# Performance work log

Hardware: AMD Instinct MI355X
Metric: run time of the kernel (lower is better)

## Reference

```python
import jax, jax.numpy as jnp
import numpy as np

DIM = 384
NUM_HEADS = 6
HEAD_DIM = DIM // NUM_HEADS
SCALE = HEAD_DIM ** -0.5


def setup_inputs() -> dict:
    key = jax.random.key(0)
    k_x, k_qkvw, k_qkvb, k_pw, k_pb = jax.random.split(key, 5)
    B, N, C = 8, 2048, DIM
    x = jax.random.normal(k_x, (B, N, C), dtype=jnp.float32)
    # nn.Linear weights stored as (out, in); apply as x @ W.T + b
    s = 1.0 / np.sqrt(C)
    qkv_w = jax.random.uniform(k_qkvw, (3 * C, C), minval=-s, maxval=s, dtype=jnp.float32)
    qkv_b = jax.random.uniform(k_qkvb, (3 * C,), minval=-s, maxval=s, dtype=jnp.float32)
    proj_w = jax.random.uniform(k_pw, (C, C), minval=-s, maxval=s, dtype=jnp.float32)
    proj_b = jax.random.uniform(k_pb, (C,), minval=-s, maxval=s, dtype=jnp.float32)
    return {"x": x, "qkv_w": qkv_w, "qkv_b": qkv_b, "proj_w": proj_w,
            "proj_b": proj_b, "h": 64, "w": 32}


def reference(x, qkv_w, qkv_b, proj_w, proj_b, h, w):
    B, N, C = x.shape
    H, D = NUM_HEADS, HEAD_DIM
    qkv = x @ qkv_w.T + qkv_b              # [B, N, 3C]
    qkv = qkv.reshape(B, N, 3, H, D)
    q = qkv[:, :, 0].transpose(0, 2, 1, 3) * SCALE  # [B, H, N, D]
    k = qkv[:, :, 1].transpose(0, 2, 1, 3)
    v = qkv[:, :, 2].transpose(0, 2, 1, 3)
    attn = jnp.einsum('bhnd,bhmd->bhnm', q, k)      # [B, H, N, N]
    attn = jax.nn.softmax(attn, axis=-1)
    out = jnp.einsum('bhnm,bhmd->bhnd', attn, v)    # [B, H, N, D]
    out = out.transpose(0, 2, 1, 3).reshape(B, N, C)
    return out @ proj_w.T + proj_b
```

## Files before the change

### kernel.cpp

```cpp
#include <hip/hip_runtime.h>

typedef __attribute__((ext_vector_type(8))) short bf16x8;
typedef __attribute__((ext_vector_type(4))) float f32x4;
typedef __attribute__((ext_vector_type(16))) float f32x16;
typedef __attribute__((ext_vector_type(4))) unsigned int u32x4;

#define DIMC 384
#define NHEADS 6
#define HDIM 64
#define BATCH 8
#define SEQ 2048
#define TOKENS (BATCH*SEQ)
#define QKV_OUT (3*DIMC)

__device__ __forceinline__ unsigned short f2bf(float f) {
  unsigned int u = __float_as_uint(f);
  u += 0x7fffu + ((u >> 16) & 1u);
  return (unsigned short)(u >> 16);
}

__device__ __forceinline__ unsigned int cvt_pk_bf16(float a, float b) {
  unsigned int r;
  asm volatile("v_cvt_pk_bf16_f32 %0, %1, %2" : "=v"(r) : "v"(a), "v"(b));
  return r;
}

__device__ __forceinline__ void async_load16(const void* g, void* l) {
  __builtin_amdgcn_global_load_lds(
      (const __attribute__((address_space(1))) unsigned int*)g,
      (__attribute__((address_space(3))) unsigned int*)l, 16, 0, 0);
}

__global__ void cast_bf16_kernel(const float* __restrict__ in,
                                 unsigned short* __restrict__ out, int n4) {
  int i = blockIdx.x * blockDim.x + threadIdx.x;
  int stride = gridDim.x * blockDim.x;
  for (; i < n4; i += stride) {
    float4 v = ((const float4*)in)[i];
    ushort4 o;
    o.x = f2bf(v.x); o.y = f2bf(v.y); o.z = f2bf(v.z); o.w = f2bf(v.w);
    ((ushort4*)out)[i] = o;
  }
}

__global__ __launch_bounds__(256) void qkv_gemm_kernel(
    const unsigned short* __restrict__ A,
    const unsigned short* __restrict__ W,
    const float* __restrict__ bias,
    unsigned short* __restrict__ Qb,
    unsigned short* __restrict__ Kb,
    unsigned short* __restrict__ Vtb) {
  __shared__ unsigned short As[128*32];
  __shared__ unsigned short Bs[128*32];
  const int tid = threadIdx.x;
  const int w = tid >> 6, l = tid & 63;
  const int wm = w >> 1, wn = w & 1;
  const int q4 = l >> 4, r15 = l & 15;
  const int m0 = blockIdx.y * 128;
  const int n0 = blockIdx.x * 128;

  f32x4 acc[4][4];
#pragma unroll
  for (int i = 0; i < 4; i++)
#pragma unroll
    for (int j = 0; j < 4; j++) acc[i][j] = f32x4{0.f, 0.f, 0.f, 0.f};

  const int arow = tid >> 2;
  const int achk = tid & 3;
  for (int kt = 0; kt < 384; kt += 32) {
    __syncthreads();
#pragma unroll
    for (int cc = 0; cc < 2; ++cc) {
      int row = cc * 64 + arow;
      async_load16(A + (size_t)(m0 + row) * 384 + kt + achk * 8,
                   (char*)As + cc * 4096 + w * 1024);
      async_load16(W + (size_t)(n0 + row) * 384 + kt + achk * 8,
                   (char*)Bs + cc * 4096 + w * 1024);
    }
    __syncthreads();
    bf16x8 a[4], b[4];
#pragma unroll
    for (int mi = 0; mi < 4; mi++)
      a[mi] = *(const bf16x8*)(As + (wm*64 + mi*16 + r15)*32 + q4*8);
#pragma unroll
    for (int ni = 0; ni < 4; ni++)
      b[ni] = *(const bf16x8*)(Bs + (wn*64 + ni*16 + r15)*32 + q4*8);
#pragma unroll
    for (int mi = 0; mi < 4; mi++)
#pragma unroll
      for (int ni = 0; ni < 4; ni++)
        acc[mi][ni] = __builtin_amdgcn_mfma_f32_16x16x32_bf16(
            a[mi], b[ni], acc[mi][ni], 0, 0, 0);
  }
  const int c3 = blockIdx.x / 3;
  const int nrel0 = (blockIdx.x % 3) * 128 + wn * 64;
  if (c3 == 2) {
#pragma unroll
    for (int ni = 0; ni < 4; ni++) {
      int ncol = nrel0 + ni*16 + r15;
      float bv = bias[n0 + wn*64 + ni*16 + r15];
      int h = ncol >> 6, d = ncol & 63;
#pragma unroll
      for (int mi = 0; mi < 4; mi++) {
        int m = m0 + wm*64 + mi*16 + 4*q4;
        int bb = m >> 11, t = m & 2047;
        ushort4 pk;
        pk.x = f2bf(acc[mi][ni][0] + bv);
        pk.y = f2bf(acc[mi][ni][1] + bv);
        pk.z = f2bf(acc[mi][ni][2] + bv);
        pk.w = f2bf(acc[mi][ni][3] + bv);
        *(ushort4*)(Vtb + ((size_t)(bb*NHEADS + h)*HDIM + d)*SEQ + t) = pk;
      }
    }
  } else {
    unsigned short* D = (c3 == 0) ? Qb : Kb;
    const float scale = (c3 == 0) ? 0.125f * 1.4426950408889634f : 1.0f;
#pragma unroll
    for (int ni = 0; ni < 4; ni++) {
      int ncol = nrel0 + ni*16 + r15;
      float bv = bias[n0 + wn*64 + ni*16 + r15];
      int h = ncol >> 6, d = ncol & 63;
#pragma unroll
      for (int mi = 0; mi < 4; mi++) {
#pragma unroll
        for (int reg = 0; reg < 4; reg++) {
          int m = m0 + wm*64 + mi*16 + 4*q4 + reg;
          int bb = m >> 11, t = m & 2047;
          float v = (acc[mi][ni][reg] + bv) * scale;
          D[((size_t)(bb*NHEADS + h)*SEQ + t)*HDIM + d] = f2bf(v);
        }
      }
    }
  }
}

__global__ __launch_bounds__(256, 3) void flash_kernel(
    const unsigned short* __restrict__ Q, const unsigned short* __restrict__ K,
    const unsigned short* __restrict__ Vt, unsigned short* __restrict__ O2) {
  __shared__ unsigned short Ks[2][64*64];
  __shared__ unsigned short Vs[2][64*64];
  const int tid = threadIdx.x;
  const int w = tid >> 6, l = tid & 63;
  const int hl = l >> 5, l31 = l & 31, l7 = l & 7;
  const int wg = blockIdx.x;
  const int logical = (wg & 7) * 96 + (wg >> 3);
  const int qt = logical & 15, bh = logical >> 4;
  const unsigned short* Qp = Q  + (size_t)bh * SEQ * HDIM;
  const unsigned short* Kp = K  + (size_t)bh * SEQ * HDIM;
  const unsigned short* Vp = Vt + (size_t)bh * HDIM * SEQ;

  const int qrow = qt*128 + w*32 + l31;
  bf16x8 qf[4];
#pragma unroll
  for (int ks = 0; ks < 4; ks++)
    qf[ks] = *(const bf16x8*)(Qp + (size_t)qrow*HDIM + ks*16 + hl*8);

  const int srow = w*8 + (l >> 3);
  const int sch  = l7 ^ (l >> 3);
  const unsigned short* Ksrc = Kp + (size_t)srow*HDIM + sch*8;
  const unsigned short* Vsrc = Vp + (size_t)srow*SEQ  + sch*8;
  char* kdst = (char*)&Ks[0][0] + w*1024;
  char* vdst = (char*)&Vs[0][0] + w*1024;

  int rdoff[4];
#pragma unroll
  for (int ks = 0; ks < 4; ks++)
    rdoff[ks] = l31*128 + (((ks*2 + hl) ^ l7) << 4);

  f32x16 o0 = {}, o1 = {};
  float l_run = 0.f;

  async_load16(Ksrc,           kdst);
  async_load16(Ksrc + 32*HDIM, kdst + 4096);
  async_load16(Vsrc,           vdst);
  async_load16(Vsrc + 32*SEQ,  vdst + 4096);

#pragma unroll 2
  for (int kt = 0; kt < 32; ++kt) {
    const int buf = kt & 1;
    const unsigned short* ksb = &Ks[buf][0];
    const unsigned short* vsb = &Vs[buf][0];
    if (kt < 31) {
      const unsigned short* ks_ = Ksrc + (size_t)(kt+1)*64*HDIM;
      const unsigned short* vs_ = Vsrc + (size_t)(kt+1)*64;
      char* kd = kdst + (buf^1)*8192;
      char* vd = vdst + (buf^1)*8192;
      async_load16(ks_,           kd);
      async_load16(ks_ + 32*HDIM, kd + 4096);
      async_load16(vs_,           vd);
      async_load16(vs_ + 32*SEQ,  vd + 4096);
      asm volatile("s_waitcnt vmcnt(4)" ::: "memory");
    } else {
      asm volatile("s_waitcnt vmcnt(0)" ::: "memory");
    }
    __builtin_amdgcn_s_barrier();
    asm volatile("" ::: "memory");

    f32x16 s0 = {}, s1 = {};
    __builtin_amdgcn_s_setprio(1);
#pragma unroll
    for (int ks = 0; ks < 4; ks++) {
      bf16x8 kf0 = *(const bf16x8*)((const char*)ksb + rdoff[ks]);
      bf16x8 kf1 = *(const bf16x8*)((const char*)ksb + 4096 + rdoff[ks]);
      s0 = __builtin_amdgcn_mfma_f32_32x32x16_bf16(kf0, qf[ks], s0, 0, 0, 0);
      s1 = __builtin_amdgcn_mfma_f32_32x32x16_bf16(kf1, qf[ks], s1, 0, 0, 0);
    }
    __builtin_amdgcn_s_setprio(0);

    unsigned int Y[2][4][2];
    float lsum = 0.f;
#pragma unroll
    for (int h = 0; h < 4; h++) {
      float a0 = __builtin_amdgcn_exp2f(s0[4*h+0]);
      float a1 = __builtin_amdgcn_exp2f(s0[4*h+1]);
      float a2 = __builtin_amdgcn_exp2f(s0[4*h+2]);
      float a3 = __builtin_amdgcn_exp2f(s0[4*h+3]);
      lsum += (a0+a1)+(a2+a3);
      Y[0][h][0] = cvt_pk_bf16(a0, a1);
      Y[0][h][1] = cvt_pk_bf16(a2, a3);
      float b0 = __builtin_amdgcn_exp2f(s1[4*h+0]);
      float b1 = __builtin_amdgcn_exp2f(s1[4*h+1]);
      float b2 = __builtin_amdgcn_exp2f(s1[4*h+2]);
      float b3 = __builtin_amdgcn_exp2f(s1[4*h+3]);
      lsum += (b0+b1)+(b2+b3);
      Y[1][h][0] = cvt_pk_bf16(b0, b1);
      Y[1][h][1] = cvt_pk_bf16(b2, b3);
    }
    l_run += lsum;

    bf16x8 pa[4];
#pragma unroll
    for (int ksl = 0; ksl < 4; ksl++) {
      const int kb = ksl >> 1, P2 = ksl & 1;
      unsigned int x0 = Y[kb][2*P2+0][0], x1 = Y[kb][2*P2+0][1];
      unsigned int y0 = Y[kb][2*P2+1][0], y1 = Y[kb][2*P2+1][1];
      asm volatile("v_permlane32_swap_b32 %0, %1" : "+v"(x0), "+v"(y0));
      asm volatile("v_permlane32_swap_b32 %0, %1" : "+v"(x1), "+v"(y1));
      u32x4 t; t[0] = x0; t[1] = x1; t[2] = y0; t[3] = y1;
      union { u32x4 u; bf16x8 b; } cvt; cvt.u = t;
      pa[ksl] = cvt.b;
    }

    __builtin_amdgcn_s_setprio(1);
#pragma unroll
    for (int ksl = 0; ksl < 4; ksl++) {
      bf16x8 vf0 = *(const bf16x8*)((const char*)vsb + rdoff[ksl]);
      bf16x8 vf1 = *(const bf16x8*)((const char*)vsb + 4096 + rdoff[ksl]);
      o0 = __builtin_amdgcn_mfma_f32_32x32x16_bf16(pa[ksl], vf0, o0, 0, 0, 0);
      o1 = __builtin_amdgcn_mfma_f32_32x32x16_bf16(pa[ksl], vf1, o1, 0, 0, 0);
    }
    __builtin_amdgcn_s_setprio(0);
    asm volatile("s_waitcnt lgkmcnt(0)" ::: "memory");
    __builtin_amdgcn_s_barrier();
    asm volatile("" ::: "memory");
  }

  l_run += __shfl_xor(l_run, 32, 64);
  const float linv = 1.0f / l_run;
  const int b = bh / NHEADS, h = bh % NHEADS;
#pragma unroll
  for (int reg = 0; reg < 16; reg++) {
    const int qr = (reg & 3) + 8*(reg >> 2) + 4*hl;
    const float lr = __shfl(linv, qr, 64);
    const int t = qt*128 + w*32 + qr;
    unsigned short* dst = O2 + ((size_t)(b*SEQ + t))*DIMC + h*HDIM;
    dst[l31]      = f2bf(o0[reg] * lr);
    dst[32 + l31] = f2bf(o1[reg] * lr);
  }
}

__global__ __launch_bounds__(256) void proj_gemm_kernel(
    const unsigned short* __restrict__ A,
    const unsigned short* __restrict__ W,
    const float* __restrict__ bias,
    float* __restrict__ out) {
  __shared__ unsigned short As[128*32];
  __shared__ unsigned short Bs[128*32];
  const int tid = threadIdx.x;
  const int w = tid >> 6, l = tid & 63;
  const int wm = w >> 1, wn = w & 1;
  const int q4 = l >> 4, r15 = l & 15;
  const int m0 = blockIdx.y * 128;
  const int n0 = blockIdx.x * 128;

  f32x4 acc[4][4];
#pragma unroll
  for (int i = 0; i < 4; i++)
#pragma unroll
    for (int j = 0; j < 4; j++) acc[i][j] = f32x4{0.f, 0.f, 0.f, 0.f};

  const int arow = tid >> 2;
  const int achk = tid & 3;
  for (int kt = 0; kt < 384; kt += 32) {
    __syncthreads();
#pragma unroll
    for (int cc = 0; cc < 2; ++cc) {
      int row = cc * 64 + arow;
      async_load16(A + (size_t)(m0 + row) * 384 + kt + achk * 8,
                   (char*)As + cc * 4096 + w * 1024);
      async_load16(W + (size_t)(n0 + row) * 384 + kt + achk * 8,
                   (char*)Bs + cc * 4096 + w * 1024);
    }
    __syncthreads();
    bf16x8 a[4], b[4];
#pragma unroll
    for (int mi = 0; mi < 4; mi++)
      a[mi] = *(const bf16x8*)(As + (wm*64 + mi*16 + r15)*32 + q4*8);
#pragma unroll
    for (int ni = 0; ni < 4; ni++)
      b[ni] = *(const bf16x8*)(Bs + (wn*64 + ni*16 + r15)*32 + q4*8);
#pragma unroll
    for (int mi = 0; mi < 4; mi++)
#pragma unroll
      for (int ni = 0; ni < 4; ni++)
        acc[mi][ni] = __builtin_amdgcn_mfma_f32_16x16x32_bf16(
            a[mi], b[ni], acc[mi][ni], 0, 0, 0);
  }
#pragma unroll
  for (int ni = 0; ni < 4; ni++) {
    int ncol = n0 + wn*64 + ni*16 + r15;
    float bv = bias[ncol];
#pragma unroll
    for (int mi = 0; mi < 4; mi++) {
#pragma unroll
      for (int reg = 0; reg < 4; reg++) {
        int m = m0 + wm*64 + mi*16 + 4*q4 + reg;
        out[(size_t)m * DIMC + ncol] = acc[mi][ni][reg] + bv;
      }
    }
  }
}

extern "C" void kernel_launch(void* const* d_in, const int* in_sizes, int n_in,
                              void* d_out, int out_size, void* d_ws, size_t ws_size,
                              hipStream_t stream) {
  const float* x      = (const float*)d_in[0];
  const float* qkv_w  = (const float*)d_in[1];
  const float* qkv_b  = (const float*)d_in[2];
  const float* proj_w = (const float*)d_in[3];
  const float* proj_b = (const float*)d_in[4];
  float* out = (float*)d_out;

  unsigned short* xbf   = (unsigned short*)d_ws;
  unsigned short* wqkv  = xbf   + (size_t)TOKENS * DIMC;
  unsigned short* wproj = wqkv  + (size_t)QKV_OUT * DIMC;
  unsigned short* Qb    = wproj + (size_t)DIMC * DIMC;
  unsigned short* Kb    = Qb    + (size_t)TOKENS * DIMC;
  unsigned short* Vtb   = Kb    + (size_t)TOKENS * DIMC;
  unsigned short* A2    = Vtb   + (size_t)TOKENS * DIMC;

  cast_bf16_kernel<<<2048, 256, 0, stream>>>(x, xbf, TOKENS * DIMC / 4);
  cast_bf16_kernel<<<432, 256, 0, stream>>>(qkv_w, wqkv, QKV_OUT * DIMC / 4);
  cast_bf16_kernel<<<144, 256, 0, stream>>>(proj_w, wproj, DIMC * DIMC / 4);
  qkv_gemm_kernel<<<dim3(9, 128), 256, 0, stream>>>(xbf, wqkv, qkv_b, Qb, Kb, Vtb);
  flash_kernel<<<768, 256, 0, stream>>>(Qb, Kb, Vtb, A2);
  proj_gemm_kernel<<<dim3(3, 128), 256, 0, stream>>>(A2, wproj, proj_b, out);
}
```

Before: 127.5 us.

## Double-buffer GEMMs, shrink flash blocks, fuse casts, retile projection

```diff
diff --git a/kernel.cpp b/kernel.cpp
--- a/kernel.cpp
+++ b/kernel.cpp
@@ -31,15 +31,26 @@
       (__attribute__((address_space(3))) unsigned int*)l, 16, 0, 0);
 }
 
-__global__ void cast_bf16_kernel(const float* __restrict__ in,
-                                 unsigned short* __restrict__ out, int n4) {
+#define N4_X   (TOKENS*DIMC/4)
+#define N4_W1  (QKV_OUT*DIMC/4)
+#define N4_W2  (DIMC*DIMC/4)
+__global__ void cast3_kernel(const float* __restrict__ x,
+                             const float* __restrict__ w1,
+                             const float* __restrict__ w2,
+                             unsigned short* __restrict__ ox,
+                             unsigned short* __restrict__ o1,
+                             unsigned short* __restrict__ o2) {
   int i = blockIdx.x * blockDim.x + threadIdx.x;
-  int stride = gridDim.x * blockDim.x;
-  for (; i < n4; i += stride) {
-    float4 v = ((const float4*)in)[i];
+  const int stride = gridDim.x * blockDim.x;
+  for (; i < N4_X + N4_W1 + N4_W2; i += stride) {
+    const float* src; unsigned short* dst; int j = i;
+    if (j < N4_X)            { src = x;  dst = ox; }
+    else if (j < N4_X+N4_W1) { j -= N4_X; src = w1; dst = o1; }
+    else                     { j -= N4_X+N4_W1; src = w2; dst = o2; }
+    float4 v = ((const float4*)src)[j];
     ushort4 o;
     o.x = f2bf(v.x); o.y = f2bf(v.y); o.z = f2bf(v.z); o.w = f2bf(v.w);
-    ((ushort4*)out)[i] = o;
+    ((ushort4*)dst)[j] = o;
   }
 }
 
@@ -50,8 +61,8 @@
     unsigned short* __restrict__ Qb,
     unsigned short* __restrict__ Kb,
     unsigned short* __restrict__ Vtb) {
-  __shared__ unsigned short As[128*32];
-  __shared__ unsigned short Bs[128*32];
+  __shared__ unsigned short As[2][128*32];
+  __shared__ unsigned short Bs[2][128*32];
   const int tid = threadIdx.x;
   const int w = tid >> 6, l = tid & 63;
   const int wm = w >> 1, wn = w & 1;
@@ -65,32 +76,49 @@
 #pragma unroll
     for (int j = 0; j < 4; j++) acc[i][j] = f32x4{0.f, 0.f, 0.f, 0.f};
 
-  const int arow = tid >> 2;
-  const int achk = tid & 3;
-  for (int kt = 0; kt < 384; kt += 32) {
-    __syncthreads();
-#pragma unroll
-    for (int cc = 0; cc < 2; ++cc) {
-      int row = cc * 64 + arow;
-      async_load16(A + (size_t)(m0 + row) * 384 + kt + achk * 8,
-                   (char*)As + cc * 4096 + w * 1024);
-      async_load16(W + (size_t)(n0 + row) * 384 + kt + achk * 8,
-                   (char*)Bs + cc * 4096 + w * 1024);
-    }
-    __syncthreads();
+  const int arow = l >> 2;
+  const int achk = l & 3;
+  const unsigned short* Asrc = A + (size_t)(m0 + w*16 + arow) * 384 + achk * 8;
+  const unsigned short* Wsrc = W + (size_t)(n0 + w*16 + arow) * 384 + achk * 8;
+
+#pragma unroll
+  for (int cc = 0; cc < 2; ++cc) {
+    async_load16(Asrc + cc*64*384, (char*)As[0] + cc*4096 + w*1024);
+    async_load16(Wsrc + cc*64*384, (char*)Bs[0] + cc*4096 + w*1024);
+  }
+
+  for (int kt = 0; kt < 12; ++kt) {
+    const int buf = kt & 1;
+    if (kt < 11) {
+#pragma unroll
+      for (int cc = 0; cc < 2; ++cc) {
+        async_load16(Asrc + (kt+1)*32 + cc*64*384, (char*)As[buf^1] + cc*4096 + w*1024);
+        async_load16(Wsrc + (kt+1)*32 + cc*64*384, (char*)Bs[buf^1] + cc*4096 + w*1024);
+      }
+      asm volatile("s_waitcnt vmcnt(4)" ::: "memory");
+    } else {
+      asm volatile("s_waitcnt vmcnt(0)" ::: "memory");
+    }
+    __builtin_amdgcn_s_barrier();
+    asm volatile("" ::: "memory");
     bf16x8 a[4], b[4];
 #pragma unroll
     for (int mi = 0; mi < 4; mi++)
-      a[mi] = *(const bf16x8*)(As + (wm*64 + mi*16 + r15)*32 + q4*8);
+      a[mi] = *(const bf16x8*)(&As[buf][(wm*64 + mi*16 + r15)*32 + q4*8]);
 #pragma unroll
     for (int ni = 0; ni < 4; ni++)
-      b[ni] = *(const bf16x8*)(Bs + (wn*64 + ni*16 + r15)*32 + q4*8);
+      b[ni] = *(const bf16x8*)(&Bs[buf][(wn*64 + ni*16 + r15)*32 + q4*8]);
+    __builtin_amdgcn_s_setprio(1);
 #pragma unroll
     for (int mi = 0; mi < 4; mi++)
 #pragma unroll
       for (int ni = 0; ni < 4; ni++)
         acc[mi][ni] = __builtin_amdgcn_mfma_f32_16x16x32_bf16(
             a[mi], b[ni], acc[mi][ni], 0, 0, 0);
+    __builtin_amdgcn_s_setprio(0);
+    asm volatile("s_waitcnt lgkmcnt(0)" ::: "memory");
+    __builtin_amdgcn_s_barrier();
+    asm volatile("" ::: "memory");
   }
   const int c3 = blockIdx.x / 3;
   const int nrel0 = (blockIdx.x % 3) * 128 + wn * 64;
@@ -134,7 +162,7 @@
   }
 }
 
-__global__ __launch_bounds__(256, 3) void flash_kernel(
+__global__ __launch_bounds__(128) void flash_kernel(
     const unsigned short* __restrict__ Q, const unsigned short* __restrict__ K,
     const unsigned short* __restrict__ Vt, unsigned short* __restrict__ O2) {
   __shared__ unsigned short Ks[2][64*64];
@@ -143,24 +171,23 @@
   const int w = tid >> 6, l = tid & 63;
   const int hl = l >> 5, l31 = l & 31, l7 = l & 7;
   const int wg = blockIdx.x;
-  const int logical = (wg & 7) * 96 + (wg >> 3);
-  const int qt = logical & 15, bh = logical >> 4;
+  const int logical = (wg & 7) * 192 + (wg >> 3);
+  const int qt = logical & 31, bh = logical >> 5;
   const unsigned short* Qp = Q  + (size_t)bh * SEQ * HDIM;
   const unsigned short* Kp = K  + (size_t)bh * SEQ * HDIM;
   const unsigned short* Vp = Vt + (size_t)bh * HDIM * SEQ;
 
-  const int qrow = qt*128 + w*32 + l31;
+  const int qrow = qt*64 + w*32 + l31;
   bf16x8 qf[4];
 #pragma unroll
   for (int ks = 0; ks < 4; ks++)
     qf[ks] = *(const bf16x8*)(Qp + (size_t)qrow*HDIM + ks*16 + hl*8);
 
-  const int srow = w*8 + (l >> 3);
-  const int sch  = l7 ^ (l >> 3);
-  const unsigned short* Ksrc = Kp + (size_t)srow*HDIM + sch*8;
-  const unsigned short* Vsrc = Vp + (size_t)srow*SEQ  + sch*8;
-  char* kdst = (char*)&Ks[0][0] + w*1024;
-  char* vdst = (char*)&Vs[0][0] + w*1024;
+  const int srow = l >> 3;
+  const int sch  = l7 ^ srow;
+  const unsigned short* Ksrc = Kp + (size_t)(w*32 + srow)*HDIM + sch*8;
+  const unsigned short* Vsrc = Vp + (size_t)(w*32 + srow)*SEQ  + sch*8;
+  const int dstoff = w*4096;
 
   int rdoff[4];
 #pragma unroll
@@ -170,10 +197,11 @@
   f32x16 o0 = {}, o1 = {};
   float l_run = 0.f;
 
-  async_load16(Ksrc,           kdst);
-  async_load16(Ksrc + 32*HDIM, kdst + 4096);
-  async_load16(Vsrc,           vdst);
-  async_load16(Vsrc + 32*SEQ,  vdst + 4096);
+#pragma unroll
+  for (int j = 0; j < 4; j++) {
+    async_load16(Ksrc + j*8*HDIM, (char*)Ks[0] + dstoff + j*1024);
+    async_load16(Vsrc + j*8*SEQ,  (char*)Vs[0] + dstoff + j*1024);
+  }
 
 #pragma unroll 2
   for (int kt = 0; kt < 32; ++kt) {
@@ -183,13 +211,12 @@
     if (kt < 31) {
       const unsigned short* ks_ = Ksrc + (size_t)(kt+1)*64*HDIM;
       const unsigned short* vs_ = Vsrc + (size_t)(kt+1)*64;
-      char* kd = kdst + (buf^1)*8192;
-      char* vd = vdst + (buf^1)*8192;
-      async_load16(ks_,           kd);
-      async_load16(ks_ + 32*HDIM, kd + 4096);
-      async_load16(vs_,           vd);
-      async_load16(vs_ + 32*SEQ,  vd + 4096);
-      asm volatile("s_waitcnt vmcnt(4)" ::: "memory");
+#pragma unroll
+      for (int j = 0; j < 4; j++) {
+        async_load16(ks_ + j*8*HDIM, (char*)Ks[buf^1] + dstoff + j*1024);
+        async_load16(vs_ + j*8*SEQ,  (char*)Vs[buf^1] + dstoff + j*1024);
+      }
+      asm volatile("s_waitcnt vmcnt(8)" ::: "memory");
     } else {
       asm volatile("s_waitcnt vmcnt(0)" ::: "memory");
     }
@@ -262,7 +289,7 @@
   for (int reg = 0; reg < 16; reg++) {
     const int qr = (reg & 3) + 8*(reg >> 2) + 4*hl;
     const float lr = __shfl(linv, qr, 64);
-    const int t = qt*128 + w*32 + qr;
+    const int t = qt*64 + w*32 + qr;
     unsigned short* dst = O2 + ((size_t)(b*SEQ + t))*DIMC + h*HDIM;
     dst[l31]      = f2bf(o0[reg] * lr);
     dst[32 + l31] = f2bf(o1[reg] * lr);
@@ -274,57 +301,71 @@
     const unsigned short* __restrict__ W,
     const float* __restrict__ bias,
     float* __restrict__ out) {
-  __shared__ unsigned short As[128*32];
-  __shared__ unsigned short Bs[128*32];
+  __shared__ unsigned short As[2][128*32];
+  __shared__ unsigned short Bs[2][64*32];
   const int tid = threadIdx.x;
   const int w = tid >> 6, l = tid & 63;
-  const int wm = w >> 1, wn = w & 1;
   const int q4 = l >> 4, r15 = l & 15;
   const int m0 = blockIdx.y * 128;
-  const int n0 = blockIdx.x * 128;
-
-  f32x4 acc[4][4];
-#pragma unroll
-  for (int i = 0; i < 4; i++)
+  const int n0 = blockIdx.x * 64;
+
+  f32x4 acc[2][4];
+#pragma unroll
+  for (int i = 0; i < 2; i++)
 #pragma unroll
     for (int j = 0; j < 4; j++) acc[i][j] = f32x4{0.f, 0.f, 0.f, 0.f};
 
-  const int arow = tid >> 2;
-  const int achk = tid & 3;
-  for (int kt = 0; kt < 384; kt += 32) {
-    __syncthreads();
-#pragma unroll
-    for (int cc = 0; cc < 2; ++cc) {
-      int row = cc * 64 + arow;
-      async_load16(A + (size_t)(m0 + row) * 384 + kt + achk * 8,
-                   (char*)As + cc * 4096 + w * 1024);
-      async_load16(W + (size_t)(n0 + row) * 384 + kt + achk * 8,
-                   (char*)Bs + cc * 4096 + w * 1024);
-    }
-    __syncthreads();
-    bf16x8 a[4], b[4];
-#pragma unroll
-    for (int mi = 0; mi < 4; mi++)
-      a[mi] = *(const bf16x8*)(As + (wm*64 + mi*16 + r15)*32 + q4*8);
+  const int arow = l >> 2;
+  const int achk = l & 3;
+  const unsigned short* Asrc = A + (size_t)(m0 + w*16 + arow) * 384 + achk * 8;
+  const unsigned short* Wsrc = W + (size_t)(n0 + w*16 + arow) * 384 + achk * 8;
+
+#pragma unroll
+  for (int cc = 0; cc < 2; ++cc)
+    async_load16(Asrc + cc*64*384, (char*)As[0] + cc*4096 + w*1024);
+  async_load16(Wsrc, (char*)Bs[0] + w*1024);
+
+  for (int kt = 0; kt < 12; ++kt) {
+    const int buf = kt & 1;
+    if (kt < 11) {
+#pragma unroll
+      for (int cc = 0; cc < 2; ++cc)
+        async_load16(Asrc + (kt+1)*32 + cc*64*384, (char*)As[buf^1] + cc*4096 + w*1024);
+      async_load16(Wsrc + (kt+1)*32, (char*)Bs[buf^1] + w*1024);
+      asm volatile("s_waitcnt vmcnt(3)" ::: "memory");
+    } else {
+      asm volatile("s_waitcnt vmcnt(0)" ::: "memory");
+    }
+    __builtin_amdgcn_s_barrier();
+    asm volatile("" ::: "memory");
+    bf16x8 a[2], b[4];
+#pragma unroll
+    for (int mi = 0; mi < 2; mi++)
+      a[mi] = *(const bf16x8*)(&As[buf][(w*32 + mi*16 + r15)*32 + q4*8]);
 #pragma unroll
     for (int ni = 0; ni < 4; ni++)
-      b[ni] = *(const bf16x8*)(Bs + (wn*64 + ni*16 + r15)*32 + q4*8);
-#pragma unroll
-    for (int mi = 0; mi < 4; mi++)
+      b[ni] = *(const bf16x8*)(&Bs[buf][(ni*16 + r15)*32 + q4*8]);
+    __builtin_amdgcn_s_setprio(1);
+#pragma unroll
+    for (int mi = 0; mi < 2; mi++)
 #pragma unroll
       for (int ni = 0; ni < 4; ni++)
         acc[mi][ni] = __builtin_amdgcn_mfma_f32_16x16x32_bf16(
             a[mi], b[ni], acc[mi][ni], 0, 0, 0);
+    __builtin_amdgcn_s_setprio(0);
+    asm volatile("s_waitcnt lgkmcnt(0)" ::: "memory");
+    __builtin_amdgcn_s_barrier();
+    asm volatile("" ::: "memory");
   }
 #pragma unroll
   for (int ni = 0; ni < 4; ni++) {
-    int ncol = n0 + wn*64 + ni*16 + r15;
+    int ncol = n0 + ni*16 + r15;
     float bv = bias[ncol];
 #pragma unroll
-    for (int mi = 0; mi < 4; mi++) {
+    for (int mi = 0; mi < 2; mi++) {
 #pragma unroll
       for (int reg = 0; reg < 4; reg++) {
-        int m = m0 + wm*64 + mi*16 + 4*q4 + reg;
+        int m = m0 + w*32 + mi*16 + 4*q4 + reg;
         out[(size_t)m * DIMC + ncol] = acc[mi][ni][reg] + bv;
       }
     }
@@ -349,10 +390,8 @@
   unsigned short* Vtb   = Kb    + (size_t)TOKENS * DIMC;
   unsigned short* A2    = Vtb   + (size_t)TOKENS * DIMC;
 
-  cast_bf16_kernel<<<2048, 256, 0, stream>>>(x, xbf, TOKENS * DIMC / 4);
-  cast_bf16_kernel<<<432, 256, 0, stream>>>(qkv_w, wqkv, QKV_OUT * DIMC / 4);
-  cast_bf16_kernel<<<144, 256, 0, stream>>>(proj_w, wproj, DIMC * DIMC / 4);
+  cast3_kernel<<<2048, 256, 0, stream>>>(x, qkv_w, proj_w, xbf, wqkv, wproj);
   qkv_gemm_kernel<<<dim3(9, 128), 256, 0, stream>>>(xbf, wqkv, qkv_b, Qb, Kb, Vtb);
-  flash_kernel<<<768, 256, 0, stream>>>(Qb, Kb, Vtb, A2);
-  proj_gemm_kernel<<<dim3(3, 128), 256, 0, stream>>>(A2, wproj, proj_b, out);
-}
+  flash_kernel<<<1536, 128, 0, stream>>>(Qb, Kb, Vtb, A2);
+  proj_gemm_kernel<<<dim3(6, 128), 256, 0, stream>>>(A2, wproj, proj_b, out);
+}
```

Result: slower. 154.0 us (+20.8%).
